# Kernel optimization log

Measured on AMD Instinct MI355X. Metric: run time of the kernel, lower is better.

The kernel has to match this reference:

```python
import jax, jax.numpy as jnp
import numpy as np
from jax import lax

LP, LQ, B, IN = 512, 256, 32, 512
H = 150  # hidden_size*2 hardcoded in module


def setup_inputs() -> dict:
    key = jax.random.key(0)
    ks = jax.random.split(key, 12)
    s = 0.05  # keep tanh/sigmoid unsaturated
    return {
        "up": jax.random.normal(ks[0], (LP, B, IN), jnp.float32),
        "uq": jax.random.normal(ks[1], (LQ, B, IN), jnp.float32),
        "v0": jax.random.normal(ks[2], (B, H), jnp.float32),
        "V": jax.random.normal(ks[3], (B, H), jnp.float32),
        "Wp": jax.random.normal(ks[4], (H, 2 * IN), jnp.float32) * s,
        "Wq": jax.random.normal(ks[5], (H, 2 * IN), jnp.float32) * s,
        "Wv": jax.random.normal(ks[6], (H, H), jnp.float32) * s,
        "Wg": jax.random.normal(ks[7], (4 * IN, 4 * IN), jnp.float32) * s,
        "W_ih": jax.random.normal(ks[8], (3 * H, 2 * IN), jnp.float32) * s,
        "W_hh": jax.random.normal(ks[9], (3 * H, H), jnp.float32) * s,
        "b_ih": jax.random.normal(ks[10], (3 * H,), jnp.float32) * s,
        "b_hh": jax.random.normal(ks[11], (3 * H,), jnp.float32) * s,
    }


def reference(up, uq, v0, V, Wp, Wq, Wv, Wg, W_ih, W_hh, b_ih, b_hh):
    in2 = up.shape[2] * 2
    Up = jnp.concatenate([up, up], axis=2)          # [lp, B, 2*in]
    Uq = jnp.concatenate([uq, uq], axis=2)          # [lq, B, 2*in]
    WqUq = jnp.einsum("qbi,hi->qbh", Uq, Wq)        # hoisted: constant over steps

    def step(v, Up_i):
        Wup = Up_i @ Wp.T                            # [B, H]
        x = jnp.tanh(Wup + WqUq + v @ Wv.T)          # [lq, B, H]
        s = jnp.einsum("qbh,bh->bq", x, V)           # attention logits [B, lq]
        a = jax.nn.softmax(s, axis=1)
        c = jnp.einsum("bq,qbi->bi", a, Uq)          # context [B, 2*in]
        r = jnp.concatenate([Up_i, c], axis=1)       # [B, 4*in]
        g = jax.nn.sigmoid(r @ Wg.T)
        r = g * r
        c_ = r[:, in2:]                              # gated context [B, 2*in]
        # GRUCell
        gi = c_ @ W_ih.T + b_ih
        gh = v @ W_hh.T + b_hh
        i_r, i_z, i_n = jnp.split(gi, 3, axis=1)
        h_r, h_z, h_n = jnp.split(gh, 3, axis=1)
        rg = jax.nn.sigmoid(i_r + h_r)
        zg = jax.nn.sigmoid(i_z + h_z)
        ng = jnp.tanh(i_n + rg * h_n)
        v_new = (1.0 - zg) * ng + zg * v
        return v_new, v_new

    _, vs = lax.scan(step, v0, Up)                   # vs: [lp, B, H]
    return vs  # dropout = identity (eval)
```

## Files before the change

kernel.cpp:

```cpp
#include <hip/hip_runtime.h>
#include <hip/hip_bf16.h>

#define AGENT __HIP_MEMORY_SCOPE_AGENT
#define RLX __ATOMIC_RELAXED
typedef unsigned long long u64t;

typedef _Float16 h2 __attribute__((ext_vector_type(2)));
union U32H2 { unsigned u; h2 h; };
__device__ __forceinline__ h2 uh(unsigned u){ U32H2 c; c.u=u; return c.h; }
__device__ __forceinline__ unsigned pk(float a, float b){
  U32H2 c; c.h = h2{(_Float16)a, (_Float16)b}; return c.u;
}
#define RCPF(x) __builtin_amdgcn_rcpf(x)

__device__ __forceinline__ float DOT2(unsigned a, unsigned b, float acc){
#if __has_builtin(__builtin_amdgcn_fdot2)
  return __builtin_amdgcn_fdot2(uh(a), uh(b), acc, false);
#else
  h2 x = uh(a), y = uh(b);
  acc = fmaf((float)x[0], (float)y[0], acc);
  return fmaf((float)x[1], (float)y[1], acc);
#endif
}
__device__ __forceinline__ float sigm(float x){ return RCPF(1.0f+__expf(-x)); }
__device__ __forceinline__ float ftanh(float x){ return 1.0f - 2.0f*RCPF(1.0f+__expf(x+x)); }

__device__ __forceinline__ void pubw(u64t* p, unsigned seq, unsigned data){
  __hip_atomic_store(p, ((u64t)seq<<32)|(u64t)data, RLX, AGENT);
}
template<int K>
__device__ __forceinline__ void waitN(const u64t* base, const int* off, unsigned seq,
                                      unsigned* out, unsigned* kf){
  long n=0;
  for(;;){
    u64t v[K]; bool ok=true;
    #pragma unroll
    for(int k=0;k<K;k++) v[k]=__hip_atomic_load(base+off[k], RLX, AGENT);
    #pragma unroll
    for(int k=0;k<K;k++) ok &= ((unsigned)(v[k]>>32)==seq);
    if(ok){
      #pragma unroll
      for(int k=0;k<K;k++) out[k]=(unsigned)v[k];
      return;
    }
    __builtin_amdgcn_s_sleep(1);
    if((++n&255)==0){
      if(__hip_atomic_load(kf,RLX,AGENT)!=0u) break;
      if(n>300000L){ __hip_atomic_store(kf,1u,RLX,AGENT); break; }
    }
  }
  #pragma unroll
  for(int k=0;k<K;k++) out[k]=0u;
}

__global__ void k_fold(const float* __restrict__ Wp, const float* __restrict__ Wq,
                       const float* __restrict__ Wg,
                       float* __restrict__ WpT, float* __restrict__ WqT,
                       float* __restrict__ WgupT, float* __restrict__ WgcT)
{
  int i0 = blockIdx.x*blockDim.x+threadIdx.x;
  int st = gridDim.x*blockDim.x;
  for(int o=i0;o<512*150;o+=st){ int h=o%150, i=o/150;
    WpT[o]=Wp[h*1024+i]+Wp[h*1024+512+i];
    WqT[o]=Wq[h*1024+i]+Wq[h*1024+512+i]; }
  for(int o=i0;o<512*1024;o+=st){ int i=o&511, j=o>>9;
    size_t rb=(size_t)(1024+j)*2048;
    WgupT[(size_t)i*1024+j]=Wg[rb+i]+Wg[rb+512+i];
    WgcT [(size_t)i*1024+j]=Wg[rb+1024+i]+Wg[rb+1536+i]; }
}

__global__ void k_fold2(const float* __restrict__ Wih,
                        const float* __restrict__ Whh, const float* __restrict__ Wv,
                        unsigned* __restrict__ WihT,
                        unsigned* __restrict__ WhhP, unsigned* __restrict__ WvU)
{
  int i0 = blockIdx.x*blockDim.x+threadIdx.x;
  int st = gridDim.x*blockDim.x;
  for(int o=i0;o<512*456;o+=st){ int k=o%456, jp=o/456;
    unsigned v = 0u;
    if(k<450) v = pk(Wih[(size_t)k*1024+2*jp], Wih[(size_t)k*1024+2*jp+1]);
    WihT[o] = v; }
  for(int o=i0;o<76*456;o+=st){ int k=o%456, p=o/456;
    float x=0.f,y=0.f;
    if(k<450){ if(2*p<150) x=Whh[k*150+2*p]; if(2*p+1<150) y=Whh[k*150+2*p+1]; }
    WhhP[o]=pk(x,y); }
  for(int o=i0;o<76*152;o+=st){ int h=o%152, p=o/152;
    float x=0.f,y=0.f;
    if(h<150){ if(2*p<150) x=Wv[h*150+2*p]; if(2*p+1<150) y=Wv[h*150+2*p+1]; }
    WvU[o]=pk(x,y); }
}

__global__ __launch_bounds__(256) void k_uqp(const float* __restrict__ uq, unsigned* __restrict__ uqP){
  __shared__ float Al[32*512];
  int b = blockIdx.x, qt = blockIdx.y, tid = threadIdx.x;
  for(int o4=tid;o4<4096;o4+=256){ int m=o4>>7, i4=o4&127;
    ((float4*)Al)[o4] = *(const float4*)&uq[(size_t)(qt*32+m)*16384 + b*512 + i4*4]; }
  __syncthreads();
  for(int o=tid;o<8192;o+=256){ int i=o>>4, p=o&15;
    uqP[((size_t)b*512+i)*128 + qt*16 + p] = pk(Al[(2*p)*512+i], Al[(2*p+1)*512+i]); }
}

template<int MODE>
__global__ __launch_bounds__(256) void k_gemm(const float* __restrict__ A,
   const float* __restrict__ WT, _Float16* __restrict__ oH, int N)
{
  __shared__ float Al[32*512];
  int mt=blockIdx.x, nt=blockIdx.y, tid=threadIdx.x;
  const float* Ab = A + (size_t)mt*16384;
  for(int o=tid;o<4096;o+=256) ((float4*)Al)[o]=((const float4*)Ab)[o];
  __syncthreads();
  int n = nt*256+tid;
  if(n>=N) return;
  float acc[32];
  #pragma unroll
  for(int m=0;m<32;m++) acc[m]=0.f;
  const float* wp = WT + n;
  #pragma unroll 2
  for(int k=0;k<512;k+=2){
    float w0 = wp[(size_t)k*N], w1 = wp[(size_t)(k+1)*N];
    #pragma unroll
    for(int m=0;m<32;m++) acc[m]=fmaf(w0, Al[m*512+k], acc[m]);
    #pragma unroll
    for(int m=0;m<32;m++) acc[m]=fmaf(w1, Al[m*512+k+1], acc[m]);
  }
  if(MODE==0){
    #pragma unroll
    for(int m=0;m<32;m++) oH[((size_t)m*512 + mt)*152 + n] = (_Float16)acc[m];
  } else if(MODE==3){
    #pragma unroll
    for(int m=0;m<32;m++) oH[((size_t)m*256 + mt)*152 + n] = (_Float16)acc[m];
  } else {
    #pragma unroll
    for(int m=0;m<32;m++) oH[((size_t)m*512 + mt)*1024 + n] = (_Float16)acc[m];
  }
}

__global__ __launch_bounds__(256) void k_gemmM(const float* __restrict__ uq,
   const float* __restrict__ WgcT, unsigned* __restrict__ Mp)
{
  __shared__ float Al[32*512];
  int b=blockIdx.x, qt=blockIdx.y, nt=blockIdx.z, tid=threadIdx.x;
  for(int o4=tid;o4<4096;o4+=256){ int m=o4>>7, i4=o4&127;
    ((float4*)Al)[o4] = *(const float4*)&uq[(size_t)(qt*32+m)*16384 + b*512 + i4*4]; }
  __syncthreads();
  int n = nt*256+tid;
  float acc[32];
  #pragma unroll
  for(int m=0;m<32;m++) acc[m]=0.f;
  const float* wp = WgcT + n;
  #pragma unroll 2
  for(int k=0;k<512;k+=2){
    float w0 = wp[(size_t)k*1024], w1 = wp[(size_t)(k+1)*1024];
    #pragma unroll
    for(int m=0;m<32;m++) acc[m]=fmaf(w0, Al[m*512+k], acc[m]);
    #pragma unroll
    for(int m=0;m<32;m++) acc[m]=fmaf(w1, Al[m*512+k+1], acc[m]);
  }
  #pragma unroll
  for(int p=0;p<16;p++)
    Mp[((size_t)b*1024 + n)*128 + qt*16 + p] = pk(acc[2*p], acc[2*p+1]);
}

__global__ void k_init(unsigned* comm){
  int i = blockIdx.x*blockDim.x + threadIdx.x;
  if(i < 66052) comm[i] = 0u;
}

struct __align__(16) SMO {
  unsigned WvU[76*152];
  unsigned WqUq[256*76];
  unsigned wup[80], vp[80];
  float V[152], v[152], w2[152], s[256], a[256];
  float gi[452], rgh[2][452], bi[452], bh[452];
};
struct __align__(16) SMW {
  unsigned M[128*257];
  unsigned a2[128], gup[128], cpr[128];
  float ccf[128], Gc[256], c_f[256], rgi[2][452];
};
union SMU { SMO o; SMW w; };

__global__ __launch_bounds__(1024) void persist(
  const unsigned* __restrict__ uqP,   const unsigned* __restrict__ Mp,
  const unsigned* __restrict__ Gup3u, const unsigned* __restrict__ Wuphu,
  const unsigned* __restrict__ WqUqhu, const unsigned* __restrict__ WihTu,
  const unsigned* __restrict__ WhhP,  const unsigned* __restrict__ WvUg,
  const float* __restrict__ v0, const float* __restrict__ Vin,
  const float* __restrict__ bih, const float* __restrict__ bhh,
  u64t* aP, u64t* giP, unsigned* kf,
  float* __restrict__ dout)
{
  extern __shared__ char smraw[];
  SMU& S = *reinterpret_cast<SMU*>(smraw);
  const int tid = threadIdx.x;
  const int bid = blockIdx.x;

  if(bid < 32){
    const int b = bid;
    for(int o=tid;o<11552;o+=1024) S.o.WvU[o]=WvUg[o];
    for(int o=tid;o<19456;o+=1024){ int q=o/76,w=o%76;
      S.o.WqUq[o]=WqUqhu[((size_t)b*256+q)*76+w]; }
    for(int o=tid;o<152;o+=1024){
      S.o.V[o]=(o<150)?Vin[b*150+o]:0.f;
      S.o.v[o]=(o<150)?v0[b*150+o]:0.f; }
    for(int o=tid;o<452;o+=1024){
      S.o.bi[o]=(o<450)?bih[o]:0.f;
      S.o.bh[o]=(o<450)?bhh[o]:0.f; }
    unsigned whh[38];
    {
      int k=tid&511, half=tid>>9;
      #pragma unroll
      for(int p=0;p<38;p++){
        int pp=half*38+p;
        whh[p] = (k<450 && pp<76)? WhhP[(size_t)pp*456+k] : 0u;
      }
    }
    __syncthreads();

    const int gib = b*904;
    for(int t=0;t<512;++t){
      if(tid<76) S.o.wup[tid]=Wuphu[((size_t)b*512+t)*76+tid];
      if(t>0){
        if(tid<225){
          int off[4]={gib+tid, gib+226+tid, gib+452+tid, gib+678+tid};
          unsigned gv[4];
          waitN<4>(giP,off,(unsigned)t,gv,kf);
          float g0=0.f,g1=0.f;
          #pragma unroll
          for(int k=0;k<4;k++){ h2 x=uh(gv[k]); g0+=(float)x[0]; g1+=(float)x[1]; }
          S.o.gi[2*tid]=g0; S.o.gi[2*tid+1]=g1;
        }
        __syncthreads();
        if(tid<150){
          float gh0=S.o.rgh[0][tid]+S.o.rgh[1][tid]+S.o.bh[tid];
          float gh1=S.o.rgh[0][150+tid]+S.o.rgh[1][150+tid]+S.o.bh[150+tid];
          float gh2=S.o.rgh[0][300+tid]+S.o.rgh[1][300+tid]+S.o.bh[300+tid];
          float rg=sigm(S.o.gi[tid]+S.o.bi[tid] + gh0);
          float zg=sigm(S.o.gi[150+tid]+S.o.bi[150+tid] + gh1);
          float ng=ftanh(S.o.gi[300+tid]+S.o.bi[300+tid] + rg*gh2);
          float vn=fmaf(zg, S.o.v[tid]-ng, ng);
          S.o.v[tid]=vn;
          dout[((size_t)(t-1)*32+b)*150+tid]=vn;
        }
        __syncthreads();
      }
      if(tid<76) S.o.vp[tid]=pk(S.o.v[2*tid], S.o.v[2*tid+1]);
      __syncthreads();
      if(tid<608){
        int h=tid>>2, qd=tid&3;
        float acc=0.f;
        if(h<150){
          #pragma unroll
          for(int p=qd*19;p<qd*19+19;p++) acc=DOT2(S.o.WvU[p*152+h], S.o.vp[p], acc);
        }
        acc+=__shfl_xor(acc,1,64); acc+=__shfl_xor(acc,2,64);
        if(h<150&&qd==0){ h2 ww=uh(S.o.wup[h>>1]); S.o.w2[h]=acc+(float)ww[h&1]; }
      }
      __syncthreads();
      {
        int q=tid>>2, hq=tid&3;
        int hp0=hq*19, hp1=(hq==3)?75:hp0+19;
        float acc=0.f;
        for(int hp=hp0;hp<hp1;hp++){
          h2 wp=uh(S.o.WqUq[q*76+hp]);
          acc=fmaf(S.o.V[2*hp],   ftanh(S.o.w2[2*hp]  +(float)wp[0]), acc);
          acc=fmaf(S.o.V[2*hp+1], ftanh(S.o.w2[2*hp+1]+(float)wp[1]), acc);
        }
        acc+=__shfl_xor(acc,1,64); acc+=__shfl_xor(acc,2,64);
        if(hq==0) S.o.s[q]=acc;
      }
      __syncthreads();
      if(tid<64){
        float x0=S.o.s[tid],x1=S.o.s[tid+64],x2=S.o.s[tid+128],x3=S.o.s[tid+192];
        float mx=fmaxf(fmaxf(x0,x1),fmaxf(x2,x3));
        #pragma unroll
        for(int o=1;o<64;o<<=1) mx=fmaxf(mx,__shfl_xor(mx,o,64));
        float e0=__expf(x0-mx),e1=__expf(x1-mx),e2=__expf(x2-mx),e3=__expf(x3-mx);
        float sm=e0+e1+e2+e3;
        #pragma unroll
        for(int o=1;o<64;o<<=1) sm+=__shfl_xor(sm,o,64);
        float rs=RCPF(sm);
        S.o.a[tid]=e0*rs; S.o.a[tid+64]=e1*rs; S.o.a[tid+128]=e2*rs; S.o.a[tid+192]=e3*rs;
      }
      __syncthreads();
      if(tid<128) pubw(aP+b*128+tid,(unsigned)(t+1), pk(S.o.a[2*tid],S.o.a[2*tid+1]));
      {
        int k=tid&511, half=tid>>9;
        if(k<450){
          float ah=0.f;
          #pragma unroll
          for(int p=0;p<38;p++) ah=DOT2(whh[p], S.o.vp[(half*38+p)<76 ? half*38+p : 0], ah);
          S.o.rgh[half][k]=ah;
        }
      }
    }
    if(tid<225){
      int off[4]={gib+tid, gib+226+tid, gib+452+tid, gib+678+tid};
      unsigned gv[4];
      waitN<4>(giP,off,512u,gv,kf);
      float g0=0.f,g1=0.f;
      #pragma unroll
      for(int k=0;k<4;k++){ h2 x=uh(gv[k]); g0+=(float)x[0]; g1+=(float)x[1]; }
      S.o.gi[2*tid]=g0; S.o.gi[2*tid+1]=g1;
    }
    __syncthreads();
    if(tid<150){
      float gh0=S.o.rgh[0][tid]+S.o.rgh[1][tid]+S.o.bh[tid];
      float gh1=S.o.rgh[0][150+tid]+S.o.rgh[1][150+tid]+S.o.bh[150+tid];
      float gh2=S.o.rgh[0][300+tid]+S.o.rgh[1][300+tid]+S.o.bh[300+tid];
      float rg=sigm(S.o.gi[tid]+S.o.bi[tid] + gh0);
      float zg=sigm(S.o.gi[150+tid]+S.o.bi[150+tid] + gh1);
      float ng=ftanh(S.o.gi[300+tid]+S.o.bi[300+tid] + rg*gh2);
      dout[((size_t)511*32+b)*150+tid]=fmaf(zg, S.o.v[tid]-ng, ng);
    }

  } else {
    const int wid = bid-32;
    const int b = wid>>2, s = wid&3;
    for(int o=tid;o<32768;o+=1024){
      int qp=o&127, jl=o>>7;
      int j = s*128 + (jl&127) + ((jl>>7)<<9);
      S.w.M[qp*257+jl] = Mp[((size_t)b*1024+j)*128+qp];
    }
    unsigned wih[64];
    {
      int k=tid&511, half=tid>>9;
      #pragma unroll
      for(int m=0;m<64;m++){
        int jpg = half*256 + s*64 + m;
        wih[m] = (k<450)? WihTu[(size_t)jpg*456+k] : 0u;
      }
    }
    __syncthreads();
    const size_t uqbase = ((size_t)b*512 + s*128)*128;
    for(int t=0;t<512;++t){
      if(tid<128){
        int wi = (tid<64)? (s*64+tid) : (256+s*64+tid-64);
        S.w.gup[tid] = Gup3u[((size_t)b*512+t)*512 + wi];
      }
      if(tid<128){
        int off[1]={b*128+tid};
        unsigned av[1];
        waitN<1>(aP,off,(unsigned)(t+1),av,kf);
        S.w.a2[tid]=av[0];
      }
      __syncthreads();
      {
        int i=tid>>3, q8=tid&7;
        float acc=0.f;
        const unsigned* up = uqP + uqbase + (size_t)i*128;
        #pragma unroll 4
        for(int kk=0;kk<16;kk++){
          int qp=kk*8+q8;
          acc=DOT2(S.w.a2[qp], up[qp], acc);
        }
        acc+=__shfl_xor(acc,1,64); acc+=__shfl_xor(acc,2,64); acc+=__shfl_xor(acc,4,64);
        if(q8==0) S.w.ccf[i]=acc;
      }
      {
        int jl=tid>>2, qc=tid&3;
        float acc=0.f;
        #pragma unroll 8
        for(int kk=0;kk<32;kk++){
          int qp=kk*4+qc;
          acc=DOT2(S.w.a2[qp], S.w.M[qp*257+jl], acc);
        }
        acc+=__shfl_xor(acc,1,64); acc+=__shfl_xor(acc,2,64);
        if(qc==0) S.w.Gc[jl]=acc;
      }
      __syncthreads();
      if(tid<256){
        h2 gv=uh(S.w.gup[tid>>1]);
        float g=sigm(S.w.Gc[tid]+(float)gv[tid&1]);
        S.w.c_f[tid]=g*S.w.ccf[tid&127];
      }
      __syncthreads();
      if(tid<128) S.w.cpr[tid]=pk(S.w.c_f[2*tid],S.w.c_f[2*tid+1]);
      __syncthreads();
      {
        int k=tid&511, half=tid>>9;
        float acc=0.f;
        #pragma unroll
        for(int m=0;m<64;m++) acc=DOT2(wih[m], S.w.cpr[half*64+m], acc);
        if(k<450) S.w.rgi[half][k]=acc;
      }
      __syncthreads();
      if(tid<225){
        float g0=S.w.rgi[0][2*tid]+S.w.rgi[1][2*tid];
        float g1=S.w.rgi[0][2*tid+1]+S.w.rgi[1][2*tid+1];
        pubw(giP + ((size_t)b*4+s)*226 + tid, (unsigned)(t+1), pk(g0,g1));
      }
    }
  }
}

extern "C" void kernel_launch(void* const* d_in, const int* in_sizes, int n_in,
                              void* d_out, int out_size, void* d_ws, size_t ws_size,
                              hipStream_t stream)
{
  const float* up  = (const float*)d_in[0];
  const float* uq  = (const float*)d_in[1];
  const float* v0  = (const float*)d_in[2];
  const float* Vm  = (const float*)d_in[3];
  const float* Wp  = (const float*)d_in[4];
  const float* Wq  = (const float*)d_in[5];
  const float* Wv  = (const float*)d_in[6];
  const float* Wg  = (const float*)d_in[7];
  const float* W_ih= (const float*)d_in[8];
  const float* W_hh= (const float*)d_in[9];
  const float* b_ih= (const float*)d_in[10];
  const float* b_hh= (const float*)d_in[11];
  float* dout = (float*)d_out;
  char* wsb = (char*)d_ws;

  size_t off = 0;
  auto alloc = [&](size_t bytes)->size_t{ size_t p = off; off = (off + bytes + 255) & ~(size_t)255; return p; };
  size_t oWgupT = alloc((size_t)512*1024*4);
  size_t oWgcT  = alloc((size_t)512*1024*4);
  size_t oWuph  = alloc((size_t)32*512*152*2);
  size_t oWqUqh = alloc((size_t)32*256*152*2);
  size_t oWihT  = alloc((size_t)512*456*4);
  size_t oWhhP  = alloc((size_t)76*456*4);
  size_t oWvU   = alloc((size_t)76*152*4);
  size_t oUqP   = alloc((size_t)32*512*128*4);
  size_t oMp    = alloc((size_t)32*1024*128*4);
  size_t oGup3  = alloc((size_t)32*512*1024*2);
  if(ws_size < off) return;

  float*    WgupT = (float*)(wsb + oWgupT);
  float*    WgcT  = (float*)(wsb + oWgcT);
  _Float16* Wuph  = (_Float16*)(wsb + oWuph);
  _Float16* WqUqh = (_Float16*)(wsb + oWqUqh);
  unsigned* WihT  = (unsigned*)(wsb + oWihT);
  unsigned* WhhP  = (unsigned*)(wsb + oWhhP);
  unsigned* WvU   = (unsigned*)(wsb + oWvU);
  unsigned* uqP   = (unsigned*)(wsb + oUqP);
  unsigned* Mp    = (unsigned*)(wsb + oMp);
  _Float16* Gup3  = (_Float16*)(wsb + oGup3);
  float* WpT = (float*)(wsb + oGup3);
  float* WqT = (float*)(wsb + oGup3 + 307456);

  u64t* comm64 = (u64t*)(wsb + oWgupT);
  u64t* aP  = comm64;
  u64t* giP = comm64 + 4096;
  unsigned* kf = (unsigned*)(comm64 + 33024);

  k_fold <<<256,256,0,stream>>>(Wp,Wq,Wg, WpT,WqT,WgupT,WgcT);
  k_fold2<<<256,256,0,stream>>>(W_ih, W_hh, Wv, WihT, WhhP, WvU);
  k_uqp  <<<dim3(32,8),256,0,stream>>>(uq, uqP);
  k_gemm<0><<<dim3(512,1),256,0,stream>>>(up, WpT, Wuph, 150);
  k_gemm<3><<<dim3(256,1),256,0,stream>>>(uq, WqT, WqUqh, 150);
  k_gemm<4><<<dim3(512,4),256,0,stream>>>(up, WgupT, Gup3, 1024);
  k_gemmM<<<dim3(32,8,4),256,0,stream>>>(uq, WgcT, Mp);
  k_init <<<65,1024,0,stream>>>((unsigned*)comm64);

  int smem = (int)sizeof(SMU);
  hipFuncSetAttribute((const void*)persist, hipFuncAttributeMaxDynamicSharedMemorySize, smem);
  const unsigned* Gup3u  = (const unsigned*)Gup3;
  const unsigned* Wuphu  = (const unsigned*)Wuph;
  const unsigned* WqUqhu = (const unsigned*)WqUqh;
  void* ka[16] = { (void*)&uqP, (void*)&Mp, (void*)&Gup3u, (void*)&Wuphu, (void*)&WqUqhu,
                   (void*)&WihT, (void*)&WhhP, (void*)&WvU,
                   (void*)&v0, (void*)&Vm, (void*)&b_ih, (void*)&b_hh,
                   (void*)&aP, (void*)&giP, (void*)&kf, (void*)&dout };
  hipLaunchCooperativeKernel((const void*)persist, dim3(160), dim3(1024), ka,
                             (unsigned)smem, stream);
}
```

Baseline: 7.468 ms.

## Merge attention blocks into workers, recomputing attention redundantly per slice

Removes the 32 dedicated attention/GRU blocks and their attention-weight handoff. Each of the 128 worker blocks now recomputes the attention, softmax and GRU update for its batch row locally, leaving one cross-block exchange per step (the gi partials) instead of two. In exchange it does the attention work four times over, and reads Wv, WqUq, W_ih and W_hh from global memory each step instead of keeping them in shared memory or registers. The spin-wait also checks the kill flag more often.

```diff
diff --git a/kernel.cpp b/kernel.cpp
--- a/kernel.cpp
+++ b/kernel.cpp
@@ -44,7 +44,7 @@
       return;
     }
     __builtin_amdgcn_s_sleep(1);
-    if((++n&255)==0){
+    if((++n&63)==0){
       if(__hip_atomic_load(kf,RLX,AGENT)!=0u) break;
       if(n>300000L){ __hip_atomic_store(kf,1u,RLX,AGENT); break; }
     }
@@ -163,22 +163,17 @@
 
 __global__ void k_init(unsigned* comm){
   int i = blockIdx.x*blockDim.x + threadIdx.x;
-  if(i < 66052) comm[i] = 0u;
-}
-
-struct __align__(16) SMO {
-  unsigned WvU[76*152];
-  unsigned WqUq[256*76];
-  unsigned wup[80], vp[80];
-  float V[152], v[152], w2[152], s[256], a[256];
-  float gi[452], rgh[2][452], bi[452], bh[452];
-};
+  if(i < 57860) comm[i] = 0u;
+}
+
 struct __align__(16) SMW {
   unsigned M[128*257];
-  unsigned a2[128], gup[128], cpr[128];
-  float ccf[128], Gc[256], c_f[256], rgi[2][452];
+  unsigned a2[128], gupl[128], cpr[128], wupl[80], vp[80];
+  float v[152], V[152], w2[152], s_[256], a_[256];
+  float ccf[128], Gc[256], c_f[256];
+  float gi[452], rgh[2][452], bi[452], bh[452];
+  float rgi[2][452];
 };
-union SMU { SMO o; SMW w; };
 
 __global__ __launch_bounds__(1024) void persist(
   const unsigned* __restrict__ uqP,   const unsigned* __restrict__ Mp,
@@ -187,113 +182,166 @@
   const unsigned* __restrict__ WhhP,  const unsigned* __restrict__ WvUg,
   const float* __restrict__ v0, const float* __restrict__ Vin,
   const float* __restrict__ bih, const float* __restrict__ bhh,
-  u64t* aP, u64t* giP, unsigned* kf,
+  u64t* giP, unsigned* kf,
   float* __restrict__ dout)
 {
   extern __shared__ char smraw[];
-  SMU& S = *reinterpret_cast<SMU*>(smraw);
+  SMW& S = *reinterpret_cast<SMW*>(smraw);
   const int tid = threadIdx.x;
-  const int bid = blockIdx.x;
-
-  if(bid < 32){
-    const int b = bid;
-    for(int o=tid;o<11552;o+=1024) S.o.WvU[o]=WvUg[o];
-    for(int o=tid;o<19456;o+=1024){ int q=o/76,w=o%76;
-      S.o.WqUq[o]=WqUqhu[((size_t)b*256+q)*76+w]; }
-    for(int o=tid;o<152;o+=1024){
-      S.o.V[o]=(o<150)?Vin[b*150+o]:0.f;
-      S.o.v[o]=(o<150)?v0[b*150+o]:0.f; }
-    for(int o=tid;o<452;o+=1024){
-      S.o.bi[o]=(o<450)?bih[o]:0.f;
-      S.o.bh[o]=(o<450)?bhh[o]:0.f; }
-    unsigned whh[38];
+  const int b = blockIdx.x>>2, s = blockIdx.x&3;
+
+  for(int o=tid;o<32768;o+=1024){
+    int qp=o&127, jl=o>>7;
+    int j = s*128 + (jl&127) + ((jl>>7)<<9);
+    S.M[qp*257+jl] = Mp[((size_t)b*1024+j)*128+qp];
+  }
+  for(int o=tid;o<152;o+=1024){
+    S.v[o]=(o<150)?v0[b*150+o]:0.f;
+    S.V[o]=(o<150)?Vin[b*150+o]:0.f; }
+  for(int o=tid;o<452;o+=1024){
+    S.bi[o]=(o<450)?bih[o]:0.f;
+    S.bh[o]=(o<450)?bhh[o]:0.f; }
+  __syncthreads();
+  if(tid<76) S.vp[tid]=pk(S.v[2*tid],S.v[2*tid+1]);
+
+  const int gib = b*904;
+  const int myslot = gib + s*226;
+  const int kk_ = tid&511, half_ = tid>>9;
+
+  for(int t=0;t<512;++t){
+    unsigned wupr = (tid<76)? Wuphu[((size_t)b*512+t)*76+tid] : 0u;
+    unsigned gupr = 0u;
+    if(tid<128){
+      int wi = (tid<64)? (s*64+tid) : (256+s*64+tid-64);
+      gupr = Gup3u[((size_t)b*512+t)*512 + wi];
+    }
+    if(t>0){
+      if(tid<225){
+        int off[4]={gib+tid, gib+226+tid, gib+452+tid, gib+678+tid};
+        unsigned gv[4];
+        waitN<4>(giP,off,(unsigned)t,gv,kf);
+        float g0=0.f,g1=0.f;
+        #pragma unroll
+        for(int k=0;k<4;k++){ h2 x=uh(gv[k]); g0+=(float)x[0]; g1+=(float)x[1]; }
+        S.gi[2*tid]=g0; S.gi[2*tid+1]=g1;
+      }
+      __syncthreads();
+      if(tid<150){
+        float gh0=S.rgh[0][tid]+S.rgh[1][tid]+S.bh[tid];
+        float gh1=S.rgh[0][150+tid]+S.rgh[1][150+tid]+S.bh[150+tid];
+        float gh2=S.rgh[0][300+tid]+S.rgh[1][300+tid]+S.bh[300+tid];
+        float rg=sigm(S.gi[tid]+S.bi[tid] + gh0);
+        float zg=sigm(S.gi[150+tid]+S.bi[150+tid] + gh1);
+        float ng=ftanh(S.gi[300+tid]+S.bi[300+tid] + rg*gh2);
+        float vn=fmaf(zg, S.v[tid]-ng, ng);
+        S.v[tid]=vn;
+        if(s==0) dout[((size_t)(t-1)*32+b)*150+tid]=vn;
+      }
+      __syncthreads();
+      if(tid<76) S.vp[tid]=pk(S.v[2*tid],S.v[2*tid+1]);
+    }
+    if(tid<76)  S.wupl[tid]=wupr;
+    if(tid<128) S.gupl[tid]=gupr;
+    __syncthreads();
+
+    if(tid<608){
+      int h=tid>>2, qd=tid&3;
+      float acc=0.f;
+      if(h<150){
+        #pragma unroll
+        for(int p=qd*19;p<qd*19+19;p++) acc=DOT2(WvUg[p*152+h], S.vp[p], acc);
+      }
+      acc+=__shfl_xor(acc,1,64); acc+=__shfl_xor(acc,2,64);
+      if(h<150&&qd==0){ h2 ww=uh(S.wupl[h>>1]); S.w2[h]=acc+(float)ww[h&1]; }
+    }
+    __syncthreads();
+
     {
-      int k=tid&511, half=tid>>9;
+      int q=tid>>2, hq=tid&3;
+      int hp0=hq*19, hp1=(hq==3)?75:hp0+19;
+      const unsigned* wq = WqUqhu + ((size_t)b*256+q)*76;
+      float acc=0.f;
+      for(int hp=hp0;hp<hp1;hp++){
+        h2 wp=uh(wq[hp]);
+        acc=fmaf(S.V[2*hp],   ftanh(S.w2[2*hp]  +(float)wp[0]), acc);
+        acc=fmaf(S.V[2*hp+1], ftanh(S.w2[2*hp+1]+(float)wp[1]), acc);
+      }
+      acc+=__shfl_xor(acc,1,64); acc+=__shfl_xor(acc,2,64);
+      if(hq==0) S.s_[q]=acc;
+    }
+    __syncthreads();
+    if(tid<64){
+      float x0=S.s_[tid],x1=S.s_[tid+64],x2=S.s_[tid+128],x3=S.s_[tid+192];
+      float mx=fmaxf(fmaxf(x0,x1),fmaxf(x2,x3));
       #pragma unroll
-      for(int p=0;p<38;p++){
-        int pp=half*38+p;
-        whh[p] = (k<450 && pp<76)? WhhP[(size_t)pp*456+k] : 0u;
-      }
-    }
-    __syncthreads();
-
-    const int gib = b*904;
-    for(int t=0;t<512;++t){
-      if(tid<76) S.o.wup[tid]=Wuphu[((size_t)b*512+t)*76+tid];
-      if(t>0){
-        if(tid<225){
-          int off[4]={gib+tid, gib+226+tid, gib+452+tid, gib+678+tid};
-          unsigned gv[4];
-          waitN<4>(giP,off,(unsigned)t,gv,kf);
-          float g0=0.f,g1=0.f;
-          #pragma unroll
-          for(int k=0;k<4;k++){ h2 x=uh(gv[k]); g0+=(float)x[0]; g1+=(float)x[1]; }
-          S.o.gi[2*tid]=g0; S.o.gi[2*tid+1]=g1;
-        }
-        __syncthreads();
-        if(tid<150){
-          float gh0=S.o.rgh[0][tid]+S.o.rgh[1][tid]+S.o.bh[tid];
-          float gh1=S.o.rgh[0][150+tid]+S.o.rgh[1][150+tid]+S.o.bh[150+tid];
-          float gh2=S.o.rgh[0][300+tid]+S.o.rgh[1][300+tid]+S.o.bh[300+tid];
-          float rg=sigm(S.o.gi[tid]+S.o.bi[tid] + gh0);
-          float zg=sigm(S.o.gi[150+tid]+S.o.bi[150+tid] + gh1);
-          float ng=ftanh(S.o.gi[300+tid]+S.o.bi[300+tid] + rg*gh2);
-          float vn=fmaf(zg, S.o.v[tid]-ng, ng);
-          S.o.v[tid]=vn;
-          dout[((size_t)(t-1)*32+b)*150+tid]=vn;
-        }
-        __syncthreads();
-      }
-      if(tid<76) S.o.vp[tid]=pk(S.o.v[2*tid], S.o.v[2*tid+1]);
-      __syncthreads();
-      if(tid<608){
-        int h=tid>>2, qd=tid&3;
-        float acc=0.f;
-        if(h<150){
-          #pragma unroll
-          for(int p=qd*19;p<qd*19+19;p++) acc=DOT2(S.o.WvU[p*152+h], S.o.vp[p], acc);
-        }
-        acc+=__shfl_xor(acc,1,64); acc+=__shfl_xor(acc,2,64);
-        if(h<150&&qd==0){ h2 ww=uh(S.o.wup[h>>1]); S.o.w2[h]=acc+(float)ww[h&1]; }
-      }
-      __syncthreads();
-      {
-        int q=tid>>2, hq=tid&3;
-        int hp0=hq*19, hp1=(hq==3)?75:hp0+19;
-        float acc=0.f;
-        for(int hp=hp0;hp<hp1;hp++){
-          h2 wp=uh(S.o.WqUq[q*76+hp]);
-          acc=fmaf(S.o.V[2*hp],   ftanh(S.o.w2[2*hp]  +(float)wp[0]), acc);
-          acc=fmaf(S.o.V[2*hp+1], ftanh(S.o.w2[2*hp+1]+(float)wp[1]), acc);
-        }
-        acc+=__shfl_xor(acc,1,64); acc+=__shfl_xor(acc,2,64);
-        if(hq==0) S.o.s[q]=acc;
-      }
-      __syncthreads();
-      if(tid<64){
-        float x0=S.o.s[tid],x1=S.o.s[tid+64],x2=S.o.s[tid+128],x3=S.o.s[tid+192];
-        float mx=fmaxf(fmaxf(x0,x1),fmaxf(x2,x3));
-        #pragma unroll
-        for(int o=1;o<64;o<<=1) mx=fmaxf(mx,__shfl_xor(mx,o,64));
-        float e0=__expf(x0-mx),e1=__expf(x1-mx),e2=__expf(x2-mx),e3=__expf(x3-mx);
-        float sm=e0+e1+e2+e3;
-        #pragma unroll
-        for(int o=1;o<64;o<<=1) sm+=__shfl_xor(sm,o,64);
-        float rs=RCPF(sm);
-        S.o.a[tid]=e0*rs; S.o.a[tid+64]=e1*rs; S.o.a[tid+128]=e2*rs; S.o.a[tid+192]=e3*rs;
-      }
-      __syncthreads();
-      if(tid<128) pubw(aP+b*128+tid,(unsigned)(t+1), pk(S.o.a[2*tid],S.o.a[2*tid+1]));
-      {
-        int k=tid&511, half=tid>>9;
-        if(k<450){
-          float ah=0.f;
-          #pragma unroll
-          for(int p=0;p<38;p++) ah=DOT2(whh[p], S.o.vp[(half*38+p)<76 ? half*38+p : 0], ah);
-          S.o.rgh[half][k]=ah;
-        }
-      }
-    }
+      for(int o=1;o<64;o<<=1) mx=fmaxf(mx,__shfl_xor(mx,o,64));
+      float e0=__expf(x0-mx),e1=__expf(x1-mx),e2=__expf(x2-mx),e3=__expf(x3-mx);
+      float sm=e0+e1+e2+e3;
+      #pragma unroll
+      for(int o=1;o<64;o<<=1) sm+=__shfl_xor(sm,o,64);
+      float rs=RCPF(sm);
+      S.a_[tid]=e0*rs; S.a_[tid+64]=e1*rs; S.a_[tid+128]=e2*rs; S.a_[tid+192]=e3*rs;
+    }
+    __syncthreads();
+    if(tid<128) S.a2[tid]=pk(S.a_[2*tid],S.a_[2*tid+1]);
+    __syncthreads();
+
+    {
+      int i=tid>>3, q8=tid&7;
+      float acc=0.f;
+      const unsigned* up = uqP + ((size_t)b*512 + s*128)*128 + (size_t)i*128;
+      #pragma unroll 4
+      for(int kk=0;kk<16;kk++){
+        int qp=kk*8+q8;
+        acc=DOT2(S.a2[qp], up[qp], acc);
+      }
+      acc+=__shfl_xor(acc,1,64); acc+=__shfl_xor(acc,2,64); acc+=__shfl_xor(acc,4,64);
+      if(q8==0) S.ccf[i]=acc;
+    }
+    {
+      int jl=tid>>2, qc=tid&3;
+      float acc=0.f;
+      #pragma unroll 8
+      for(int kk=0;kk<32;kk++){
+        int qp=kk*4+qc;
+        acc=DOT2(S.a2[qp], S.M[qp*257+jl], acc);
+      }
+      acc+=__shfl_xor(acc,1,64); acc+=__shfl_xor(acc,2,64);
+      if(qc==0) S.Gc[jl]=acc;
+    }
+    __syncthreads();
+    if(tid<256){
+      h2 gv=uh(S.gupl[tid>>1]);
+      float g=sigm(S.Gc[tid]+(float)gv[tid&1]);
+      S.c_f[tid]=g*S.ccf[tid&127];
+    }
+    __syncthreads();
+    if(tid<128) S.cpr[tid]=pk(S.c_f[2*tid],S.c_f[2*tid+1]);
+    __syncthreads();
+
+    if(kk_<450){
+      float acc=0.f;
+      #pragma unroll 8
+      for(int m=0;m<64;m++){
+        int jpg = half_*256 + s*64 + m;
+        acc=DOT2(WihTu[(size_t)jpg*456+kk_], S.cpr[half_*64+m], acc);
+      }
+      S.rgi[half_][kk_]=acc;
+    }
+    __syncthreads();
+    if(tid<225){
+      float g0=S.rgi[0][2*tid]+S.rgi[1][2*tid];
+      float g1=S.rgi[0][2*tid+1]+S.rgi[1][2*tid+1];
+      pubw(giP + myslot + tid, (unsigned)(t+1), pk(g0,g1));
+    }
+    if(kk_<450){
+      float ah=0.f;
+      int p0=half_*38, p1=half_?76:38;
+      for(int p=p0;p<p1;p++) ah=DOT2(WhhP[p*456+kk_], S.vp[p], ah);
+      S.rgh[half_][kk_]=ah;
+    }
+  }
+  if(s==0){
     if(tid<225){
       int off[4]={gib+tid, gib+226+tid, gib+452+tid, gib+678+tid};
       unsigned gv[4];
@@ -301,95 +349,17 @@
       float g0=0.f,g1=0.f;
       #pragma unroll
       for(int k=0;k<4;k++){ h2 x=uh(gv[k]); g0+=(float)x[0]; g1+=(float)x[1]; }
-      S.o.gi[2*tid]=g0; S.o.gi[2*tid+1]=g1;
+      S.gi[2*tid]=g0; S.gi[2*tid+1]=g1;
     }
     __syncthreads();
     if(tid<150){
-      float gh0=S.o.rgh[0][tid]+S.o.rgh[1][tid]+S.o.bh[tid];
-      float gh1=S.o.rgh[0][150+tid]+S.o.rgh[1][150+tid]+S.o.bh[150+tid];
-      float gh2=S.o.rgh[0][300+tid]+S.o.rgh[1][300+tid]+S.o.bh[300+tid];
-      float rg=sigm(S.o.gi[tid]+S.o.bi[tid] + gh0);
-      float zg=sigm(S.o.gi[150+tid]+S.o.bi[150+tid] + gh1);
-      float ng=ftanh(S.o.gi[300+tid]+S.o.bi[300+tid] + rg*gh2);
-      dout[((size_t)511*32+b)*150+tid]=fmaf(zg, S.o.v[tid]-ng, ng);
-    }
-
-  } else {
-    const int wid = bid-32;
-    const int b = wid>>2, s = wid&3;
-    for(int o=tid;o<32768;o+=1024){
-      int qp=o&127, jl=o>>7;
-      int j = s*128 + (jl&127) + ((jl>>7)<<9);
-      S.w.M[qp*257+jl] = Mp[((size_t)b*1024+j)*128+qp];
-    }
-    unsigned wih[64];
-    {
-      int k=tid&511, half=tid>>9;
-      #pragma unroll
-      for(int m=0;m<64;m++){
-        int jpg = half*256 + s*64 + m;
-        wih[m] = (k<450)? WihTu[(size_t)jpg*456+k] : 0u;
-      }
-    }
-    __syncthreads();
-    const size_t uqbase = ((size_t)b*512 + s*128)*128;
-    for(int t=0;t<512;++t){
-      if(tid<128){
-        int wi = (tid<64)? (s*64+tid) : (256+s*64+tid-64);
-        S.w.gup[tid] = Gup3u[((size_t)b*512+t)*512 + wi];
-      }
-      if(tid<128){
-        int off[1]={b*128+tid};
-        unsigned av[1];
-        waitN<1>(aP,off,(unsigned)(t+1),av,kf);
-        S.w.a2[tid]=av[0];
-      }
-      __syncthreads();
-      {
-        int i=tid>>3, q8=tid&7;
-        float acc=0.f;
-        const unsigned* up = uqP + uqbase + (size_t)i*128;
-        #pragma unroll 4
-        for(int kk=0;kk<16;kk++){
-          int qp=kk*8+q8;
-          acc=DOT2(S.w.a2[qp], up[qp], acc);
-        }
-        acc+=__shfl_xor(acc,1,64); acc+=__shfl_xor(acc,2,64); acc+=__shfl_xor(acc,4,64);
-        if(q8==0) S.w.ccf[i]=acc;
-      }
-      {
-        int jl=tid>>2, qc=tid&3;
-        float acc=0.f;
-        #pragma unroll 8
-        for(int kk=0;kk<32;kk++){
-          int qp=kk*4+qc;
-          acc=DOT2(S.w.a2[qp], S.w.M[qp*257+jl], acc);
-        }
-        acc+=__shfl_xor(acc,1,64); acc+=__shfl_xor(acc,2,64);
-        if(qc==0) S.w.Gc[jl]=acc;
-      }
-      __syncthreads();
-      if(tid<256){
-        h2 gv=uh(S.w.gup[tid>>1]);
-        float g=sigm(S.w.Gc[tid]+(float)gv[tid&1]);
-        S.w.c_f[tid]=g*S.w.ccf[tid&127];
-      }
-      __syncthreads();
-      if(tid<128) S.w.cpr[tid]=pk(S.w.c_f[2*tid],S.w.c_f[2*tid+1]);
-      __syncthreads();
-      {
-        int k=tid&511, half=tid>>9;
-        float acc=0.f;
-        #pragma unroll
-        for(int m=0;m<64;m++) acc=DOT2(wih[m], S.w.cpr[half*64+m], acc);
-        if(k<450) S.w.rgi[half][k]=acc;
-      }
-      __syncthreads();
-      if(tid<225){
-        float g0=S.w.rgi[0][2*tid]+S.w.rgi[1][2*tid];
-        float g1=S.w.rgi[0][2*tid+1]+S.w.rgi[1][2*tid+1];
-        pubw(giP + ((size_t)b*4+s)*226 + tid, (unsigned)(t+1), pk(g0,g1));
-      }
+      float gh0=S.rgh[0][tid]+S.rgh[1][tid]+S.bh[tid];
+      float gh1=S.rgh[0][150+tid]+S.rgh[1][150+tid]+S.bh[150+tid];
+      float gh2=S.rgh[0][300+tid]+S.rgh[1][300+tid]+S.bh[300+tid];
+      float rg=sigm(S.gi[tid]+S.bi[tid] + gh0);
+      float zg=sigm(S.gi[150+tid]+S.bi[150+tid] + gh1);
+      float ng=ftanh(S.gi[300+tid]+S.bi[300+tid] + rg*gh2);
+      dout[((size_t)511*32+b)*150+tid]=fmaf(zg, S.v[tid]-ng, ng);
     }
   }
 }
@@ -441,9 +411,8 @@
   float* WqT = (float*)(wsb + oGup3 + 307456);
 
   u64t* comm64 = (u64t*)(wsb + oWgupT);
-  u64t* aP  = comm64;
-  u64t* giP = comm64 + 4096;
-  unsigned* kf = (unsigned*)(comm64 + 33024);
+  u64t* giP = comm64;
+  unsigned* kf = (unsigned*)(comm64 + 28928);
 
   k_fold <<<256,256,0,stream>>>(Wp,Wq,Wg, WpT,WqT,WgupT,WgcT);
   k_fold2<<<256,256,0,stream>>>(W_ih, W_hh, Wv, WihT, WhhP, WvU);
@@ -452,17 +421,17 @@
   k_gemm<3><<<dim3(256,1),256,0,stream>>>(uq, WqT, WqUqh, 150);
   k_gemm<4><<<dim3(512,4),256,0,stream>>>(up, WgupT, Gup3, 1024);
   k_gemmM<<<dim3(32,8,4),256,0,stream>>>(uq, WgcT, Mp);
-  k_init <<<65,1024,0,stream>>>((unsigned*)comm64);
-
-  int smem = (int)sizeof(SMU);
+  k_init <<<57,1024,0,stream>>>((unsigned*)comm64);
+
+  int smem = (int)sizeof(SMW);
   hipFuncSetAttribute((const void*)persist, hipFuncAttributeMaxDynamicSharedMemorySize, smem);
   const unsigned* Gup3u  = (const unsigned*)Gup3;
   const unsigned* Wuphu  = (const unsigned*)Wuph;
   const unsigned* WqUqhu = (const unsigned*)WqUqh;
-  void* ka[16] = { (void*)&uqP, (void*)&Mp, (void*)&Gup3u, (void*)&Wuphu, (void*)&WqUqhu,
+  void* ka[15] = { (void*)&uqP, (void*)&Mp, (void*)&Gup3u, (void*)&Wuphu, (void*)&WqUqhu,
                    (void*)&WihT, (void*)&WhhP, (void*)&WvU,
                    (void*)&v0, (void*)&Vm, (void*)&b_ih, (void*)&b_hh,
-                   (void*)&aP, (void*)&giP, (void*)&kf, (void*)&dout };
-  hipLaunchCooperativeKernel((const void*)persist, dim3(160), dim3(1024), ka,
+                   (void*)&giP, (void*)&kf, (void*)&dout };
+  hipLaunchCooperativeKernel((const void*)persist, dim3(128), dim3(1024), ka,
                              (unsigned)smem, stream);
 }
```

Measured after the change: 19.39 ms. 160% more time.

## Stream GRU weights from global with row-major uint4 loads instead of registers

Applied to the files above, without the earlier changes.

The W_hh and W_ih slices that each thread previously held in registers (38 and 64 unsigned values) are now read from global or L2 every step. The weights are stored row-major per output k so each thread loads them as contiguous uint4 vectors. The uqP context loads are vectorised to uint4, the M shared-memory row pitch changes from 257 to 265, and the gi publish slots are interleaved per thread (tid*4+s) so the consumer reads four adjacent slots. The aim is to cut register pressure in the 1024-thread persistent kernel, at the cost of repeated cache reads on the serial recurrent path.

```diff
diff --git a/kernel.cpp b/kernel.cpp
--- a/kernel.cpp
+++ b/kernel.cpp
@@ -71,19 +71,17 @@
 
 __global__ void k_fold2(const float* __restrict__ Wih,
                         const float* __restrict__ Whh, const float* __restrict__ Wv,
-                        unsigned* __restrict__ WihT,
-                        unsigned* __restrict__ WhhP, unsigned* __restrict__ WvU)
+                        unsigned* __restrict__ WihKJ,
+                        unsigned* __restrict__ WhhKP, unsigned* __restrict__ WvU)
 {
   int i0 = blockIdx.x*blockDim.x+threadIdx.x;
   int st = gridDim.x*blockDim.x;
-  for(int o=i0;o<512*456;o+=st){ int k=o%456, jp=o/456;
-    unsigned v = 0u;
-    if(k<450) v = pk(Wih[(size_t)k*1024+2*jp], Wih[(size_t)k*1024+2*jp+1]);
-    WihT[o] = v; }
-  for(int o=i0;o<76*456;o+=st){ int k=o%456, p=o/456;
-    float x=0.f,y=0.f;
-    if(k<450){ if(2*p<150) x=Whh[k*150+2*p]; if(2*p+1<150) y=Whh[k*150+2*p+1]; }
-    WhhP[o]=pk(x,y); }
+  for(int o=i0;o<450*512;o+=st){ int jp=o&511, k=o>>9;
+    WihKJ[o] = pk(Wih[(size_t)k*1024+2*jp], Wih[(size_t)k*1024+2*jp+1]); }
+  for(int o=i0;o<450*76;o+=st){ int p=o%76, k=o/76;
+    float x = (2*p<150)? Whh[k*150+2*p] : 0.f;
+    float y = (2*p+1<150)? Whh[k*150+2*p+1] : 0.f;
+    WhhKP[o]=pk(x,y); }
   for(int o=i0;o<76*152;o+=st){ int h=o%152, p=o/152;
     float x=0.f,y=0.f;
     if(h<150){ if(2*p<150) x=Wv[h*150+2*p]; if(2*p+1<150) y=Wv[h*150+2*p+1]; }
@@ -174,7 +172,7 @@
   float gi[452], rgh[2][452], bi[452], bh[452];
 };
 struct __align__(16) SMW {
-  unsigned M[128*257];
+  unsigned M[128*265];
   unsigned a2[128], gup[128], cpr[128];
   float ccf[128], Gc[256], c_f[256], rgi[2][452];
 };
@@ -183,8 +181,8 @@
 __global__ __launch_bounds__(1024) void persist(
   const unsigned* __restrict__ uqP,   const unsigned* __restrict__ Mp,
   const unsigned* __restrict__ Gup3u, const unsigned* __restrict__ Wuphu,
-  const unsigned* __restrict__ WqUqhu, const unsigned* __restrict__ WihTu,
-  const unsigned* __restrict__ WhhP,  const unsigned* __restrict__ WvUg,
+  const unsigned* __restrict__ WqUqhu, const unsigned* __restrict__ WihKJ,
+  const unsigned* __restrict__ WhhKP,  const unsigned* __restrict__ WvUg,
   const float* __restrict__ v0, const float* __restrict__ Vin,
   const float* __restrict__ bih, const float* __restrict__ bhh,
   u64t* aP, u64t* giP, unsigned* kf,
@@ -206,15 +204,6 @@
     for(int o=tid;o<452;o+=1024){
       S.o.bi[o]=(o<450)?bih[o]:0.f;
       S.o.bh[o]=(o<450)?bhh[o]:0.f; }
-    unsigned whh[38];
-    {
-      int k=tid&511, half=tid>>9;
-      #pragma unroll
-      for(int p=0;p<38;p++){
-        int pp=half*38+p;
-        whh[p] = (k<450 && pp<76)? WhhP[(size_t)pp*456+k] : 0u;
-      }
-    }
     __syncthreads();
 
     const int gib = b*904;
@@ -222,7 +211,7 @@
       if(tid<76) S.o.wup[tid]=Wuphu[((size_t)b*512+t)*76+tid];
       if(t>0){
         if(tid<225){
-          int off[4]={gib+tid, gib+226+tid, gib+452+tid, gib+678+tid};
+          int off[4]={gib+tid*4, gib+tid*4+1, gib+tid*4+2, gib+tid*4+3};
           unsigned gv[4];
           waitN<4>(giP,off,(unsigned)t,gv,kf);
           float g0=0.f,g1=0.f;
@@ -287,15 +276,16 @@
       {
         int k=tid&511, half=tid>>9;
         if(k<450){
+          const unsigned* wh = WhhKP + (size_t)k*76 + half*38;
           float ah=0.f;
           #pragma unroll
-          for(int p=0;p<38;p++) ah=DOT2(whh[p], S.o.vp[(half*38+p)<76 ? half*38+p : 0], ah);
+          for(int p=0;p<38;p++) ah=DOT2(wh[p], S.o.vp[half*38+p], ah);
           S.o.rgh[half][k]=ah;
         }
       }
     }
     if(tid<225){
-      int off[4]={gib+tid, gib+226+tid, gib+452+tid, gib+678+tid};
+      int off[4]={gib+tid*4, gib+tid*4+1, gib+tid*4+2, gib+tid*4+3};
       unsigned gv[4];
       waitN<4>(giP,off,512u,gv,kf);
       float g0=0.f,g1=0.f;
@@ -320,19 +310,10 @@
     for(int o=tid;o<32768;o+=1024){
       int qp=o&127, jl=o>>7;
       int j = s*128 + (jl&127) + ((jl>>7)<<9);
-      S.w.M[qp*257+jl] = Mp[((size_t)b*1024+j)*128+qp];
-    }
-    unsigned wih[64];
-    {
-      int k=tid&511, half=tid>>9;
-      #pragma unroll
-      for(int m=0;m<64;m++){
-        int jpg = half*256 + s*64 + m;
-        wih[m] = (k<450)? WihTu[(size_t)jpg*456+k] : 0u;
-      }
+      S.w.M[qp*265+jl] = Mp[((size_t)b*1024+j)*128+qp];
     }
     __syncthreads();
-    const size_t uqbase = ((size_t)b*512 + s*128)*128;
+    const int gib = b*904;
     for(int t=0;t<512;++t){
       if(tid<128){
         int wi = (tid<64)? (s*64+tid) : (256+s*64+tid-64);
@@ -348,11 +329,13 @@
       {
         int i=tid>>3, q8=tid&7;
         float acc=0.f;
-        const unsigned* up = uqP + uqbase + (size_t)i*128;
-        #pragma unroll 4
-        for(int kk=0;kk<16;kk++){
-          int qp=kk*8+q8;
-          acc=DOT2(S.w.a2[qp], up[qp], acc);
+        const uint4* up4 = (const uint4*)(uqP + ((size_t)b*512 + s*128 + i)*128 + q8*16);
+        #pragma unroll
+        for(int c4=0;c4<4;c4++){
+          uint4 u = up4[c4];
+          int qb = q8*16 + c4*4;
+          acc=DOT2(S.w.a2[qb],u.x,acc); acc=DOT2(S.w.a2[qb+1],u.y,acc);
+          acc=DOT2(S.w.a2[qb+2],u.z,acc); acc=DOT2(S.w.a2[qb+3],u.w,acc);
         }
         acc+=__shfl_xor(acc,1,64); acc+=__shfl_xor(acc,2,64); acc+=__shfl_xor(acc,4,64);
         if(q8==0) S.w.ccf[i]=acc;
@@ -363,7 +346,7 @@
         #pragma unroll 8
         for(int kk=0;kk<32;kk++){
           int qp=kk*4+qc;
-          acc=DOT2(S.w.a2[qp], S.w.M[qp*257+jl], acc);
+          acc=DOT2(S.w.a2[qp], S.w.M[qp*265+jl], acc);
         }
         acc+=__shfl_xor(acc,1,64); acc+=__shfl_xor(acc,2,64);
         if(qc==0) S.w.Gc[jl]=acc;
@@ -379,16 +362,24 @@
       __syncthreads();
       {
         int k=tid&511, half=tid>>9;
-        float acc=0.f;
-        #pragma unroll
-        for(int m=0;m<64;m++) acc=DOT2(wih[m], S.w.cpr[half*64+m], acc);
-        if(k<450) S.w.rgi[half][k]=acc;
+        if(k<450){
+          const uint4* wr = (const uint4*)(WihKJ + (size_t)k*512 + half*256 + s*64);
+          float acc=0.f;
+          #pragma unroll
+          for(int m4=0;m4<16;m4++){
+            uint4 w = wr[m4];
+            int mb = half*64 + m4*4;
+            acc=DOT2(w.x,S.w.cpr[mb],acc);   acc=DOT2(w.y,S.w.cpr[mb+1],acc);
+            acc=DOT2(w.z,S.w.cpr[mb+2],acc); acc=DOT2(w.w,S.w.cpr[mb+3],acc);
+          }
+          S.w.rgi[half][k]=acc;
+        }
       }
       __syncthreads();
       if(tid<225){
         float g0=S.w.rgi[0][2*tid]+S.w.rgi[1][2*tid];
         float g1=S.w.rgi[0][2*tid+1]+S.w.rgi[1][2*tid+1];
-        pubw(giP + ((size_t)b*4+s)*226 + tid, (unsigned)(t+1), pk(g0,g1));
+        pubw(giP + gib + tid*4 + s, (unsigned)(t+1), pk(g0,g1));
       }
     }
   }
@@ -419,8 +410,8 @@
   size_t oWgcT  = alloc((size_t)512*1024*4);
   size_t oWuph  = alloc((size_t)32*512*152*2);
   size_t oWqUqh = alloc((size_t)32*256*152*2);
-  size_t oWihT  = alloc((size_t)512*456*4);
-  size_t oWhhP  = alloc((size_t)76*456*4);
+  size_t oWihKJ = alloc((size_t)450*512*4);
+  size_t oWhhKP = alloc((size_t)450*76*4);
   size_t oWvU   = alloc((size_t)76*152*4);
   size_t oUqP   = alloc((size_t)32*512*128*4);
   size_t oMp    = alloc((size_t)32*1024*128*4);
@@ -431,8 +422,8 @@
   float*    WgcT  = (float*)(wsb + oWgcT);
   _Float16* Wuph  = (_Float16*)(wsb + oWuph);
   _Float16* WqUqh = (_Float16*)(wsb + oWqUqh);
-  unsigned* WihT  = (unsigned*)(wsb + oWihT);
-  unsigned* WhhP  = (unsigned*)(wsb + oWhhP);
+  unsigned* WihKJ = (unsigned*)(wsb + oWihKJ);
+  unsigned* WhhKP = (unsigned*)(wsb + oWhhKP);
   unsigned* WvU   = (unsigned*)(wsb + oWvU);
   unsigned* uqP   = (unsigned*)(wsb + oUqP);
   unsigned* Mp    = (unsigned*)(wsb + oMp);
@@ -446,7 +437,7 @@
   unsigned* kf = (unsigned*)(comm64 + 33024);
 
   k_fold <<<256,256,0,stream>>>(Wp,Wq,Wg, WpT,WqT,WgupT,WgcT);
-  k_fold2<<<256,256,0,stream>>>(W_ih, W_hh, Wv, WihT, WhhP, WvU);
+  k_fold2<<<256,256,0,stream>>>(W_ih, W_hh, Wv, WihKJ, WhhKP, WvU);
   k_uqp  <<<dim3(32,8),256,0,stream>>>(uq, uqP);
   k_gemm<0><<<dim3(512,1),256,0,stream>>>(up, WpT, Wuph, 150);
   k_gemm<3><<<dim3(256,1),256,0,stream>>>(uq, WqT, WqUqh, 150);
@@ -460,7 +451,7 @@
   const unsigned* Wuphu  = (const unsigned*)Wuph;
   const unsigned* WqUqhu = (const unsigned*)WqUqh;
   void* ka[16] = { (void*)&uqP, (void*)&Mp, (void*)&Gup3u, (void*)&Wuphu, (void*)&WqUqhu,
-                   (void*)&WihT, (void*)&WhhP, (void*)&WvU,
+                   (void*)&WihKJ, (void*)&WhhKP, (void*)&WvU,
                    (void*)&v0, (void*)&Vm, (void*)&b_ih, (void*)&b_hh,
                    (void*)&aP, (void*)&giP, (void*)&kf, (void*)&dout };
   hipLaunchCooperativeKernel((const void*)persist, dim3(160), dim3(1024), ka,
```

Result: slower. 10.63 ms (+42.4%).

## Stream recurrent weights from global instead of registers and merge GRU/gate phases

Applied to the files above, without the earlier changes.

Drops the register-resident copies of W_hh and W_ih (38 and 64 registers per thread) and reads those weights from global/L2 on every step, which should ease register pressure in the 1024-thread persistent kernel. The GRU update is fused with packing v into fp16 pairs, and the gate+pack stage is merged into one pass, removing two block barriers per step. Softmax probabilities are published straight from registers via a lane shuffle, skipping a shared-memory round trip and a barrier. The M row stride changes from 257 to 265. The cost is extra global-memory traffic and latency on the serial critical path of every step.

```diff
diff --git a/kernel.cpp b/kernel.cpp
--- a/kernel.cpp
+++ b/kernel.cpp
@@ -170,13 +170,13 @@
   unsigned WvU[76*152];
   unsigned WqUq[256*76];
   unsigned wup[80], vp[80];
-  float V[152], v[152], w2[152], s[256], a[256];
+  float V[152], v[152], w2[152], s[256];
   float gi[452], rgh[2][452], bi[452], bh[452];
 };
 struct __align__(16) SMW {
-  unsigned M[128*257];
+  unsigned M[128*265];
   unsigned a2[128], gup[128], cpr[128];
-  float ccf[128], Gc[256], c_f[256], rgi[2][452];
+  float ccf[128], Gc[256], rgi[2][452];
 };
 union SMU { SMO o; SMW w; };
 
@@ -206,15 +206,8 @@
     for(int o=tid;o<452;o+=1024){
       S.o.bi[o]=(o<450)?bih[o]:0.f;
       S.o.bh[o]=(o<450)?bhh[o]:0.f; }
-    unsigned whh[38];
-    {
-      int k=tid&511, half=tid>>9;
-      #pragma unroll
-      for(int p=0;p<38;p++){
-        int pp=half*38+p;
-        whh[p] = (k<450 && pp<76)? WhhP[(size_t)pp*456+k] : 0u;
-      }
-    }
+    __syncthreads();
+    if(tid<76) S.o.vp[tid]=pk(S.o.v[2*tid], S.o.v[2*tid+1]);
     __syncthreads();
 
     const int gib = b*904;
@@ -231,20 +224,28 @@
           S.o.gi[2*tid]=g0; S.o.gi[2*tid+1]=g1;
         }
         __syncthreads();
-        if(tid<150){
-          float gh0=S.o.rgh[0][tid]+S.o.rgh[1][tid]+S.o.bh[tid];
-          float gh1=S.o.rgh[0][150+tid]+S.o.rgh[1][150+tid]+S.o.bh[150+tid];
-          float gh2=S.o.rgh[0][300+tid]+S.o.rgh[1][300+tid]+S.o.bh[300+tid];
-          float rg=sigm(S.o.gi[tid]+S.o.bi[tid] + gh0);
-          float zg=sigm(S.o.gi[150+tid]+S.o.bi[150+tid] + gh1);
-          float ng=ftanh(S.o.gi[300+tid]+S.o.bi[300+tid] + rg*gh2);
-          float vn=fmaf(zg, S.o.v[tid]-ng, ng);
-          S.o.v[tid]=vn;
-          dout[((size_t)(t-1)*32+b)*150+tid]=vn;
-        }
-        __syncthreads();
-      }
-      if(tid<76) S.o.vp[tid]=pk(S.o.v[2*tid], S.o.v[2*tid+1]);
+        if(tid<75){
+          int h0=2*tid, h1=h0+1;
+          float gh00=S.o.rgh[0][h0]+S.o.rgh[1][h0]+S.o.bh[h0];
+          float gh10=S.o.rgh[0][150+h0]+S.o.rgh[1][150+h0]+S.o.bh[150+h0];
+          float gh20=S.o.rgh[0][300+h0]+S.o.rgh[1][300+h0]+S.o.bh[300+h0];
+          float rg0=sigm(S.o.gi[h0]+S.o.bi[h0]+gh00);
+          float zg0=sigm(S.o.gi[150+h0]+S.o.bi[150+h0]+gh10);
+          float ng0=ftanh(S.o.gi[300+h0]+S.o.bi[300+h0]+rg0*gh20);
+          float vn0=fmaf(zg0, S.o.v[h0]-ng0, ng0);
+          float gh01=S.o.rgh[0][h1]+S.o.rgh[1][h1]+S.o.bh[h1];
+          float gh11=S.o.rgh[0][150+h1]+S.o.rgh[1][150+h1]+S.o.bh[150+h1];
+          float gh21=S.o.rgh[0][300+h1]+S.o.rgh[1][300+h1]+S.o.bh[300+h1];
+          float rg1=sigm(S.o.gi[h1]+S.o.bi[h1]+gh01);
+          float zg1=sigm(S.o.gi[150+h1]+S.o.bi[150+h1]+gh11);
+          float ng1=ftanh(S.o.gi[300+h1]+S.o.bi[300+h1]+rg1*gh21);
+          float vn1=fmaf(zg1, S.o.v[h1]-ng1, ng1);
+          S.o.v[h0]=vn0; S.o.v[h1]=vn1;
+          S.o.vp[tid]=pk(vn0,vn1);
+          dout[((size_t)(t-1)*32+b)*150+h0]=vn0;
+          dout[((size_t)(t-1)*32+b)*150+h1]=vn1;
+        }
+      }
       __syncthreads();
       if(tid<608){
         int h=tid>>2, qd=tid&3;
@@ -280,16 +281,23 @@
         #pragma unroll
         for(int o=1;o<64;o<<=1) sm+=__shfl_xor(sm,o,64);
         float rs=RCPF(sm);
-        S.o.a[tid]=e0*rs; S.o.a[tid+64]=e1*rs; S.o.a[tid+128]=e2*rs; S.o.a[tid+192]=e3*rs;
-      }
-      __syncthreads();
-      if(tid<128) pubw(aP+b*128+tid,(unsigned)(t+1), pk(S.o.a[2*tid],S.o.a[2*tid+1]));
+        float a0=e0*rs, a1=e1*rs, a2v=e2*rs, a3=e3*rs;
+        float y0=__shfl_xor(a0,1,64), y1=__shfl_xor(a1,1,64);
+        float y2=__shfl_xor(a2v,1,64), y3=__shfl_xor(a3,1,64);
+        if(!(tid&1)){
+          int w=tid>>1;
+          pubw(aP+b*128+w,    (unsigned)(t+1), pk(a0,y0));
+          pubw(aP+b*128+32+w, (unsigned)(t+1), pk(a1,y1));
+          pubw(aP+b*128+64+w, (unsigned)(t+1), pk(a2v,y2));
+          pubw(aP+b*128+96+w, (unsigned)(t+1), pk(a3,y3));
+        }
+      }
       {
         int k=tid&511, half=tid>>9;
         if(k<450){
           float ah=0.f;
-          #pragma unroll
-          for(int p=0;p<38;p++) ah=DOT2(whh[p], S.o.vp[(half*38+p)<76 ? half*38+p : 0], ah);
+          int p0=half*38, p1=half?76:38;
+          for(int p=p0;p<p1;p++) ah=DOT2(WhhP[p*456+k], S.o.vp[p], ah);
           S.o.rgh[half][k]=ah;
         }
       }
@@ -320,29 +328,19 @@
     for(int o=tid;o<32768;o+=1024){
       int qp=o&127, jl=o>>7;
       int j = s*128 + (jl&127) + ((jl>>7)<<9);
-      S.w.M[qp*257+jl] = Mp[((size_t)b*1024+j)*128+qp];
-    }
-    unsigned wih[64];
-    {
-      int k=tid&511, half=tid>>9;
-      #pragma unroll
-      for(int m=0;m<64;m++){
-        int jpg = half*256 + s*64 + m;
-        wih[m] = (k<450)? WihTu[(size_t)jpg*456+k] : 0u;
-      }
+      S.w.M[qp*265+jl] = Mp[((size_t)b*1024+j)*128+qp];
     }
     __syncthreads();
     const size_t uqbase = ((size_t)b*512 + s*128)*128;
     for(int t=0;t<512;++t){
       if(tid<128){
         int wi = (tid<64)? (s*64+tid) : (256+s*64+tid-64);
-        S.w.gup[tid] = Gup3u[((size_t)b*512+t)*512 + wi];
-      }
-      if(tid<128){
+        unsigned gupr = Gup3u[((size_t)b*512+t)*512 + wi];
         int off[1]={b*128+tid};
         unsigned av[1];
         waitN<1>(aP,off,(unsigned)(t+1),av,kf);
         S.w.a2[tid]=av[0];
+        S.w.gup[tid]=gupr;
       }
       __syncthreads();
       {
@@ -363,26 +361,30 @@
         #pragma unroll 8
         for(int kk=0;kk<32;kk++){
           int qp=kk*4+qc;
-          acc=DOT2(S.w.a2[qp], S.w.M[qp*257+jl], acc);
+          acc=DOT2(S.w.a2[qp], S.w.M[qp*265+jl], acc);
         }
         acc+=__shfl_xor(acc,1,64); acc+=__shfl_xor(acc,2,64);
         if(qc==0) S.w.Gc[jl]=acc;
       }
       __syncthreads();
-      if(tid<256){
-        h2 gv=uh(S.w.gup[tid>>1]);
-        float g=sigm(S.w.Gc[tid]+(float)gv[tid&1]);
-        S.w.c_f[tid]=g*S.w.ccf[tid&127];
-      }
-      __syncthreads();
-      if(tid<128) S.w.cpr[tid]=pk(S.w.c_f[2*tid],S.w.c_f[2*tid+1]);
+      if(tid<128){
+        h2 gv=uh(S.w.gup[tid]);
+        float c0=sigm(S.w.Gc[2*tid]  +(float)gv[0])*S.w.ccf[(2*tid)&127];
+        float c1=sigm(S.w.Gc[2*tid+1]+(float)gv[1])*S.w.ccf[(2*tid+1)&127];
+        S.w.cpr[tid]=pk(c0,c1);
+      }
       __syncthreads();
       {
         int k=tid&511, half=tid>>9;
         float acc=0.f;
-        #pragma unroll
-        for(int m=0;m<64;m++) acc=DOT2(wih[m], S.w.cpr[half*64+m], acc);
-        if(k<450) S.w.rgi[half][k]=acc;
+        if(k<450){
+          #pragma unroll 8
+          for(int m=0;m<64;m++){
+            int jpg = half*256 + s*64 + m;
+            acc=DOT2(WihTu[(size_t)jpg*456+k], S.w.cpr[half*64+m], acc);
+          }
+          S.w.rgi[half][k]=acc;
+        }
       }
       __syncthreads();
       if(tid<225){
```

After: 6.873 ms. -8.0%, faster.
